# Kernel optimization log

Measured on AMD Instinct MI355X. Metric: run time of the kernel, lower is better.

Reference implementation:

```python
import jax, jax.numpy as jnp
import numpy as np

N = 100000
E = 1600000
D_IN = 128
D_OUT = 128
HEADS = 4
C = D_OUT // HEADS  # per-head channels = 32
NEG_SLOPE = 0.2
EPS_SOFTMAX = 1e-16
EPS_LN = 1e-5


def setup_inputs() -> dict:
    key = jax.random.key(0)
    ks = jax.random.split(key, 10)
    x = jax.random.normal(ks[0], (N, D_IN), dtype=jnp.float32)
    edge_index = jax.random.randint(ks[1], (2, E), 0, N, dtype=jnp.int64)
    s = 1.0 / np.sqrt(D_IN)
    W = jax.random.normal(ks[2], (D_IN, HEADS * C), dtype=jnp.float32) * s
    att_src = jax.random.normal(ks[3], (HEADS, C), dtype=jnp.float32) * (1.0 / np.sqrt(C))
    att_dst = jax.random.normal(ks[4], (HEADS, C), dtype=jnp.float32) * (1.0 / np.sqrt(C))
    gat_bias = jax.random.normal(ks[5], (D_OUT,), dtype=jnp.float32) * 0.02
    skip_W = jax.random.normal(ks[6], (D_IN, D_OUT), dtype=jnp.float32) * s
    skip_b = jax.random.normal(ks[7], (D_OUT,), dtype=jnp.float32) * 0.02
    ln_g = jnp.ones((D_OUT,), dtype=jnp.float32)
    ln_b = jnp.zeros((D_OUT,), dtype=jnp.float32)
    return {"x": x, "edge_index": edge_index, "W": W, "att_src": att_src,
            "att_dst": att_dst, "gat_bias": gat_bias, "skip_W": skip_W,
            "skip_b": skip_b, "ln_g": ln_g, "ln_b": ln_b}


def _gat_edge_conv(x, src, dst, W, att_src, att_dst, gat_bias, skip_W, skip_b, ln_g, ln_b):
    n = x.shape[0]
    h = (x @ W).reshape(n, HEADS, C)                      # [N,H,C]
    a_s = jnp.einsum('nhc,hc->nh', h, att_src)            # [N,H]
    a_d = jnp.einsum('nhc,hc->nh', h, att_dst)            # [N,H]
    e = jax.nn.leaky_relu(a_s[src] + a_d[dst], NEG_SLOPE)  # [E,H]
    # segment softmax over incoming edges of each dst node
    m = jax.ops.segment_max(e, dst, num_segments=n)        # [N,H]
    p = jnp.exp(e - m[dst])
    z = jax.ops.segment_sum(p, dst, num_segments=n)        # [N,H]
    alpha = p / (z[dst] + EPS_SOFTMAX)                     # [E,H]
    msg = h[src] * alpha[:, :, None]                       # [E,H,C]
    out = jax.ops.segment_sum(msg, dst, num_segments=n)    # [N,H,C]
    out = out.reshape(n, HEADS * C) + gat_bias
    out = out + x @ skip_W + skip_b
    mu = out.mean(-1, keepdims=True)
    var = ((out - mu) ** 2).mean(-1, keepdims=True)
    return (out - mu) * jax.lax.rsqrt(var + EPS_LN) * ln_g + ln_b


def reference(x, edge_index, W, att_src, att_dst, gat_bias, skip_W, skip_b, ln_g, ln_b):
    n = x.shape[0]
    loops = jnp.arange(n, dtype=edge_index.dtype)          # PyG GATConv add_self_loops=True
    src = jnp.concatenate([edge_index[0], loops])
    dst = jnp.concatenate([edge_index[1], loops])
    return _gat_edge_conv(x, src, dst, W, att_src, att_dst, gat_bias, skip_W, skip_b, ln_g, ln_b)
```

## Files before the change

kernel.cpp:

```cpp
#include <hip/hip_runtime.h>
#include <hip/hip_bf16.h>

#define D 128
#define HEADS 4
#define NEG_SLOPE 0.2f

typedef __attribute__((ext_vector_type(8))) short short8;
typedef __attribute__((ext_vector_type(4))) float f32x4;

__device__ __forceinline__ float lrelu(float v) {
    return v > 0.f ? v : NEG_SLOPE * v;
}

__device__ __forceinline__ short f2bf(float v) {
    __hip_bfloat16 b = __float2bfloat16(v);
    short s;
    __builtin_memcpy(&s, &b, 2);
    return s;
}

__device__ __forceinline__ float bf_lo(unsigned int u) {
    return __uint_as_float(u << 16);
}
__device__ __forceinline__ float bf_hi(unsigned int u) {
    return __uint_as_float(u & 0xffff0000u);
}

__global__ __launch_bounds__(256)
void wprep_kernel(const float* __restrict__ W, const float* __restrict__ S,
                  short* __restrict__ wsT) {
    int idx = blockIdx.x * 256 + threadIdx.x;
    int nn = idx >> 7, k = idx & 127;
    float v = (nn < 128) ? W[k * D + nn] : S[k * D + (nn - 128)];
    wsT[idx] = f2bf(v);
}

#define LDSPAD 136
__global__ __launch_bounds__(512, 4)
void gemm_mfma_kernel(const float* __restrict__ x, const short* __restrict__ wsT,
                      const float* __restrict__ skip_b, const float* __restrict__ gat_bias,
                      unsigned short* __restrict__ hb, unsigned short* __restrict__ baseb,
                      int n) {
    __shared__ short xs[64][LDSPAD];
    const int t = threadIdx.x;
    const int row0 = blockIdx.x * 64;
    #pragma unroll
    for (int i = 0; i < 4; ++i) {
        int f = t + 512 * i;
        int row = f >> 5, c4 = (f & 31) * 4;
        float4 v = make_float4(0.f, 0.f, 0.f, 0.f);
        if (row0 + row < n) v = *(const float4*)&x[(size_t)(row0 + row) * D + c4];
        short4 s4;
        s4.x = f2bf(v.x); s4.y = f2bf(v.y); s4.z = f2bf(v.z); s4.w = f2bf(v.w);
        *(short4*)&xs[row][c4] = s4;
    }
    __syncthreads();
    const int wv = t >> 6, lane = t & 63;
    const int lo = lane & 15, hi = lane >> 4;
    const int wr = wv >> 2;
    const int wc = wv & 3;
    f32x4 acc[2][4] = {};
    #pragma unroll
    for (int k0 = 0; k0 < 128; k0 += 32) {
        const int kk = k0 + hi * 8;
        short8 a0 = *(const short8*)&xs[wr * 32 + lo][kk];
        short8 a1 = *(const short8*)&xs[wr * 32 + 16 + lo][kk];
        #pragma unroll
        for (int nt = 0; nt < 4; ++nt) {
            short8 b = *(const short8*)&wsT[(wc * 64 + nt * 16 + lo) * D + kk];
            acc[0][nt] = __builtin_amdgcn_mfma_f32_16x16x32_bf16(a0, b, acc[0][nt], 0, 0, 0);
            acc[1][nt] = __builtin_amdgcn_mfma_f32_16x16x32_bf16(a1, b, acc[1][nt], 0, 0, 0);
        }
    }
    #pragma unroll
    for (int nt = 0; nt < 4; ++nt) {
        const int cc = wc * 64 + nt * 16 + lo;
        const bool isH = cc < 128;
        const float bb = isH ? 0.f : (skip_b[cc - 128] + gat_bias[cc - 128]);
        unsigned short* dst = isH ? hb : baseb;
        const int c = isH ? cc : cc - 128;
        #pragma unroll
        for (int mt = 0; mt < 2; ++mt) {
            const int rbase = row0 + wr * 32 + mt * 16 + hi * 4;
            #pragma unroll
            for (int reg = 0; reg < 4; ++reg) {
                const int r = rbase + reg;
                if (r < n) dst[(size_t)r * D + c] = (unsigned short)f2bf(acc[mt][nt][reg] + bb);
            }
        }
    }
}

__global__ __launch_bounds__(128)
void attn_proj_kernel(const unsigned short* __restrict__ hb,
                      const float* __restrict__ att_src, const float* __restrict__ att_dst,
                      float* __restrict__ a_s, float* __restrict__ a_d, int n) {
    const int i = blockIdx.x;
    const int j = threadIdx.x;
    float hv = __uint_as_float(((unsigned int)hb[(size_t)i * D + j]) << 16);
    float ps = hv * att_src[j];
    float pd = hv * att_dst[j];
    #pragma unroll
    for (int off = 16; off; off >>= 1) {
        ps += __shfl_down(ps, off, 32);
        pd += __shfl_down(pd, off, 32);
    }
    __shared__ float sa[HEADS], sd[HEADS];
    if ((j & 31) == 0) { sa[j >> 5] = ps; sd[j >> 5] = pd; }
    __syncthreads();
    if (j < HEADS) {
        a_s[i * HEADS + j] = sa[j];
        a_d[i * HEADS + j] = sd[j];
    }
}

#define BEPT 16
#define BCHUNK (256 * BEPT)

__global__ __launch_bounds__(256)
void bhist_kernel(const int* __restrict__ ei, int* __restrict__ bcnt, int E_, int nb) {
    __shared__ int hist[512];
    const int t = threadIdx.x;
    for (int q = t; q < 512; q += 256) hist[q] = 0;
    __syncthreads();
    const int base = blockIdx.x * BCHUNK;
    #pragma unroll
    for (int i = 0; i < BEPT; ++i) {
        int e = base + i * 256 + t;
        if (e < E_) atomicAdd(&hist[ei[E_ + e] >> 8], 1);
    }
    __syncthreads();
    for (int q = t; q < nb; q += 256) {
        int v = hist[q];
        if (v) atomicAdd(&bcnt[q], v);
    }
}

__global__ __launch_bounds__(512)
void bscan_kernel(const int* __restrict__ bcnt, int* __restrict__ bbase,
                  int* __restrict__ woffA, int nb) {
    __shared__ int ts[512];
    const int t = threadIdx.x;
    int v = (t < nb) ? bcnt[t] : 0;
    ts[t] = v;
    __syncthreads();
    for (int off = 1; off < 512; off <<= 1) {
        int x = (t >= off) ? ts[t - off] : 0;
        __syncthreads();
        ts[t] += x;
        __syncthreads();
    }
    if (t < nb) {
        int ex = ts[t] - v;
        bbase[t] = ex;
        woffA[t] = ex;
        if (t == nb - 1) bbase[nb] = ts[t];
    }
}

__global__ __launch_bounds__(256)
void binA_kernel(const int* __restrict__ ei, int* __restrict__ woffA,
                 int2* __restrict__ pairs, int E_, int nb) {
    __shared__ int hist[512];
    __shared__ int gbase[512];
    const int t = threadIdx.x;
    for (int q = t; q < 512; q += 256) hist[q] = 0;
    __syncthreads();
    int sv[BEPT], dv[BEPT], rk[BEPT];
    const int base = blockIdx.x * BCHUNK;
    #pragma unroll
    for (int i = 0; i < BEPT; ++i) {
        int e = base + i * 256 + t;
        if (e < E_) {
            sv[i] = ei[e];
            dv[i] = ei[E_ + e];
            rk[i] = atomicAdd(&hist[dv[i] >> 8], 1);
        } else {
            sv[i] = -1;
        }
    }
    __syncthreads();
    for (int q = t; q < nb; q += 256) {
        int v = hist[q];
        gbase[q] = v ? atomicAdd(&woffA[q], v) : 0;
    }
    __syncthreads();
    #pragma unroll
    for (int i = 0; i < BEPT; ++i) {
        if (sv[i] >= 0) {
            int pos = gbase[dv[i] >> 8] + rk[i];
            pairs[pos] = make_int2(sv[i], dv[i]);
        }
    }
}

__global__ __launch_bounds__(256)
void binB_kernel(const int2* __restrict__ pairs, const int* __restrict__ bbase,
                 int* __restrict__ cnt, int* __restrict__ offs,
                 int* __restrict__ ssrc, int n) {
    __shared__ int nhist[256];
    __shared__ int sc[256];
    __shared__ int run[256];
    const int b = blockIdx.x;
    const int t = threadIdx.x;
    const int node0 = b << 8;
    const int sbeg = bbase[b], send = bbase[b + 1];
    nhist[t] = 0;
    __syncthreads();
    for (int e = sbeg + t; e < send; e += 256)
        atomicAdd(&nhist[pairs[e].y - node0], 1);
    __syncthreads();
    int v = nhist[t];
    sc[t] = v;
    __syncthreads();
    for (int off = 1; off < 256; off <<= 1) {
        int x = (t >= off) ? sc[t - off] : 0;
        __syncthreads();
        sc[t] += x;
        __syncthreads();
    }
    int ex = sc[t] - v;
    run[t] = sbeg + ex;
    if (node0 + t < n) {
        cnt[node0 + t] = v;
        offs[node0 + t] = sbeg + ex;
    }
    __syncthreads();
    for (int e = sbeg + t; e < send; e += 256) {
        int2 p = pairs[e];
        int pos = atomicAdd(&run[p.y - node0], 1);
        ssrc[pos] = p.x;
    }
}

__global__ __launch_bounds__(256)
void gather_kernel(const int* __restrict__ offs, const int* __restrict__ cnt,
                   const int* __restrict__ ssrc, const float* __restrict__ a_s,
                   const float* __restrict__ a_d, const unsigned int* __restrict__ hb2,
                   const unsigned int* __restrict__ baseb2,
                   const float* __restrict__ ln_g, const float* __restrict__ ln_b,
                   float* __restrict__ out, int n) {
    const int lane = threadIdx.x & 63;
    const int i = blockIdx.x * 4 + (threadIdx.x >> 6);
    if (i >= n) return;
    const int e4 = lane >> 2, h4 = lane & 3;
    const int hA = lane >> 4;
    const float as_h4 = a_s[i * HEADS + h4];
    const float ad_h4 = a_d[i * HEADS + h4];
    float qself = __expf(lrelu(as_h4 + ad_h4));
    float zacc = (e4 == 0) ? qself : 0.f;
    float qselfA = __shfl(qself, hA, 64);
    unsigned int hv0 = hb2[(size_t)i * 64 + lane];
    float acc0 = bf_lo(hv0) * qselfA;
    float acc1 = bf_hi(hv0) * qselfA;
    const int o = offs[i];
    const int c = cnt[i];
    for (int k0 = 0; k0 < c; k0 += 16) {
        const int rem = c - k0;
        int sidx = 0;
        float q = 0.f;
        if (e4 < rem) {
            sidx = ssrc[o + k0 + e4];
            q = __expf(lrelu(a_s[sidx * HEADS + h4] + ad_h4));
        }
        zacc += q;
        const int m = rem < 16 ? rem : 16;
        int ee = 0;
        for (; ee + 4 <= m; ee += 4) {
            const int s0 = __shfl(sidx, (ee + 0) * 4, 64);
            const int s1 = __shfl(sidx, (ee + 1) * 4, 64);
            const int s2 = __shfl(sidx, (ee + 2) * 4, 64);
            const int s3 = __shfl(sidx, (ee + 3) * 4, 64);
            const float q0 = __shfl(q, (ee + 0) * 4 + hA, 64);
            const float q1 = __shfl(q, (ee + 1) * 4 + hA, 64);
            const float q2 = __shfl(q, (ee + 2) * 4 + hA, 64);
            const float q3 = __shfl(q, (ee + 3) * 4 + hA, 64);
            const unsigned int v0 = hb2[(size_t)s0 * 64 + lane];
            const unsigned int v1 = hb2[(size_t)s1 * 64 + lane];
            const unsigned int v2 = hb2[(size_t)s2 * 64 + lane];
            const unsigned int v3 = hb2[(size_t)s3 * 64 + lane];
            acc0 = fmaf(bf_lo(v0), q0, acc0);
            acc1 = fmaf(bf_hi(v0), q0, acc1);
            acc0 = fmaf(bf_lo(v1), q1, acc0);
            acc1 = fmaf(bf_hi(v1), q1, acc1);
            acc0 = fmaf(bf_lo(v2), q2, acc0);
            acc1 = fmaf(bf_hi(v2), q2, acc1);
            acc0 = fmaf(bf_lo(v3), q3, acc0);
            acc1 = fmaf(bf_hi(v3), q3, acc1);
        }
        for (; ee < m; ++ee) {
            const int s = __shfl(sidx, ee * 4, 64);
            const float qq = __shfl(q, ee * 4 + hA, 64);
            const unsigned int v = hb2[(size_t)s * 64 + lane];
            acc0 = fmaf(bf_lo(v), qq, acc0);
            acc1 = fmaf(bf_hi(v), qq, acc1);
        }
    }
    #pragma unroll
    for (int off = 4; off < 64; off <<= 1) zacc += __shfl_xor(zacc, off, 64);
    const float zz = __shfl(zacc, hA, 64);
    const float rz = 1.f / (zz + 1e-16f);
    const unsigned int bv = baseb2[(size_t)i * 64 + lane];
    float v0 = acc0 * rz + bf_lo(bv);
    float v1 = acc1 * rz + bf_hi(bv);
    float s1 = v0 + v1, s2 = v0 * v0 + v1 * v1;
    #pragma unroll
    for (int off = 1; off < 64; off <<= 1) {
        s1 += __shfl_xor(s1, off, 64);
        s2 += __shfl_xor(s2, off, 64);
    }
    const float mu = s1 * (1.f / 128.f);
    const float var = s2 * (1.f / 128.f) - mu * mu;
    const float r = rsqrtf(var + 1e-5f);
    const float2 g2 = *(const float2*)&ln_g[2 * lane];
    const float2 b2 = *(const float2*)&ln_b[2 * lane];
    float2 o2;
    o2.x = (v0 - mu) * r * g2.x + b2.x;
    o2.y = (v1 - mu) * r * g2.y + b2.y;
    *(float2*)&out[(size_t)i * D + 2 * lane] = o2;
}

extern "C" void kernel_launch(void* const* d_in, const int* in_sizes, int n_in,
                              void* d_out, int out_size, void* d_ws, size_t ws_size,
                              hipStream_t stream) {
    const float* x        = (const float*)d_in[0];
    const int*   ei       = (const int*)d_in[1];
    const float* W        = (const float*)d_in[2];
    const float* att_src  = (const float*)d_in[3];
    const float* att_dst  = (const float*)d_in[4];
    const float* gat_bias = (const float*)d_in[5];
    const float* skip_W   = (const float*)d_in[6];
    const float* skip_b   = (const float*)d_in[7];
    const float* ln_g     = (const float*)d_in[8];
    const float* ln_b     = (const float*)d_in[9];
    float* out = (float*)d_out;

    const int n  = in_sizes[0] / D;
    const int E_ = in_sizes[1] / 2;
    const int nb = (n + 255) >> 8;

    char* p = (char*)d_ws;
    auto carve = [&p](size_t bytes) {
        char* r = p;
        p += (bytes + 255) & ~(size_t)255;
        return r;
    };
    short* wsT            = (short*)carve(32768 * sizeof(short));
    unsigned short* hb    = (unsigned short*)carve((size_t)n * D * 2);
    unsigned short* baseb = (unsigned short*)carve((size_t)n * D * 2);
    float* a_s            = (float*)carve((size_t)n * HEADS * 4);
    float* a_d            = (float*)carve((size_t)n * HEADS * 4);
    int*   cnt            = (int*)carve((size_t)n * 4);
    int*   offs           = (int*)carve((size_t)n * 4);
    int*   bcnt           = (int*)carve(512 * 4);
    int*   bbase          = (int*)carve(513 * 4);
    int*   woffA          = (int*)carve(512 * 4);
    int*   ssrc           = (int*)carve((size_t)E_ * 4);
    int2*  pairs          = (int2*)carve((size_t)E_ * 8);

    hipMemsetAsync(bcnt, 0, 512 * sizeof(int), stream);

    wprep_kernel<<<128, 256, 0, stream>>>(W, skip_W, wsT);
    gemm_mfma_kernel<<<(n + 63) / 64, 512, 0, stream>>>(x, wsT, skip_b, gat_bias,
                                                        hb, baseb, n);
    attn_proj_kernel<<<n, 128, 0, stream>>>(hb, att_src, att_dst, a_s, a_d, n);
    const int BA = (E_ + BCHUNK - 1) / BCHUNK;
    bhist_kernel<<<BA, 256, 0, stream>>>(ei, bcnt, E_, nb);
    bscan_kernel<<<1, 512, 0, stream>>>(bcnt, bbase, woffA, nb);
    binA_kernel<<<BA, 256, 0, stream>>>(ei, woffA, pairs, E_, nb);
    binB_kernel<<<nb, 256, 0, stream>>>(pairs, bbase, cnt, offs, ssrc, n);
    gather_kernel<<<(n + 3) / 4, 256, 0, stream>>>(offs, cnt, ssrc, a_s, a_d,
                                                   (const unsigned int*)hb,
                                                   (const unsigned int*)baseb,
                                                   ln_g, ln_b, out, n);
}
```

Before: 319.5 us.

## Split wave into two half-wave edge streams with 8-byte gathers; batch attention projection

The gather kernel now has each half-wave (32 lanes) process alternate edges. Each lane loads 8 bytes (4 bf16 channels) per neighbour row, so one wavefront fetches two neighbour rows per load instruction, and the halves are combined with a cross-half shuffle at the end. The attention projection kernel now processes 4 nodes per 256-thread block, one wave per node, using xor-shuffles instead of shared memory and a syncthreads. This cuts load-instruction count and per-edge shuffle overhead in the memory-bound gather. The cost is an extra reduction across the two halves, and only half the lanes stay active for the final store.

```diff
diff --git a/kernel.cpp b/kernel.cpp
--- a/kernel.cpp
+++ b/kernel.cpp
@@ -91,26 +91,27 @@
     }
 }
 
-__global__ __launch_bounds__(128)
-void attn_proj_kernel(const unsigned short* __restrict__ hb,
+__global__ __launch_bounds__(256)
+void attn_proj_kernel(const unsigned int* __restrict__ hb2,
                       const float* __restrict__ att_src, const float* __restrict__ att_dst,
                       float* __restrict__ a_s, float* __restrict__ a_d, int n) {
-    const int i = blockIdx.x;
-    const int j = threadIdx.x;
-    float hv = __uint_as_float(((unsigned int)hb[(size_t)i * D + j]) << 16);
-    float ps = hv * att_src[j];
-    float pd = hv * att_dst[j];
-    #pragma unroll
-    for (int off = 16; off; off >>= 1) {
-        ps += __shfl_down(ps, off, 32);
-        pd += __shfl_down(pd, off, 32);
-    }
-    __shared__ float sa[HEADS], sd[HEADS];
-    if ((j & 31) == 0) { sa[j >> 5] = ps; sd[j >> 5] = pd; }
-    __syncthreads();
-    if (j < HEADS) {
-        a_s[i * HEADS + j] = sa[j];
-        a_d[i * HEADS + j] = sd[j];
+    const int lane = threadIdx.x & 63;
+    const int i = blockIdx.x * 4 + (threadIdx.x >> 6);
+    if (i >= n) return;
+    unsigned int u = hb2[(size_t)i * 64 + lane];
+    float h0 = bf_lo(u), h1 = bf_hi(u);
+    float2 as2 = ((const float2*)att_src)[lane];
+    float2 ad2 = ((const float2*)att_dst)[lane];
+    float ps = h0 * as2.x + h1 * as2.y;
+    float pd = h0 * ad2.x + h1 * ad2.y;
+    #pragma unroll
+    for (int off = 1; off < 16; off <<= 1) {
+        ps += __shfl_xor(ps, off, 64);
+        pd += __shfl_xor(pd, off, 64);
+    }
+    if ((lane & 15) == 0) {
+        a_s[i * HEADS + (lane >> 4)] = ps;
+        a_d[i * HEADS + (lane >> 4)] = pd;
     }
 }
 
@@ -236,23 +237,31 @@
 __global__ __launch_bounds__(256)
 void gather_kernel(const int* __restrict__ offs, const int* __restrict__ cnt,
                    const int* __restrict__ ssrc, const float* __restrict__ a_s,
-                   const float* __restrict__ a_d, const unsigned int* __restrict__ hb2,
-                   const unsigned int* __restrict__ baseb2,
+                   const float* __restrict__ a_d, const uint2* __restrict__ hb4,
+                   const uint2* __restrict__ baseb4,
                    const float* __restrict__ ln_g, const float* __restrict__ ln_b,
                    float* __restrict__ out, int n) {
     const int lane = threadIdx.x & 63;
     const int i = blockIdx.x * 4 + (threadIdx.x >> 6);
     if (i >= n) return;
     const int e4 = lane >> 2, h4 = lane & 3;
-    const int hA = lane >> 4;
+    const int l31 = lane & 31;
+    const int myhead = l31 >> 3;
+    const int esel = (lane < 32) ? 0 : 1;
     const float as_h4 = a_s[i * HEADS + h4];
     const float ad_h4 = a_d[i * HEADS + h4];
     float qself = __expf(lrelu(as_h4 + ad_h4));
     float zacc = (e4 == 0) ? qself : 0.f;
-    float qselfA = __shfl(qself, hA, 64);
-    unsigned int hv0 = hb2[(size_t)i * 64 + lane];
-    float acc0 = bf_lo(hv0) * qselfA;
-    float acc1 = bf_hi(hv0) * qselfA;
+    float acc0, acc1, acc2, acc3;
+    {
+        uint2 u = hb4[(size_t)i * 32 + l31];
+        float qs = __shfl(qself, myhead, 64);
+        float w = (lane < 32) ? qs : 0.f;
+        acc0 = bf_lo(u.x) * w;
+        acc1 = bf_hi(u.x) * w;
+        acc2 = bf_lo(u.y) * w;
+        acc3 = bf_hi(u.y) * w;
+    }
     const int o = offs[i];
     const int c = cnt[i];
     for (int k0 = 0; k0 < c; k0 += 16) {
@@ -266,58 +275,84 @@
         zacc += q;
         const int m = rem < 16 ? rem : 16;
         int ee = 0;
-        for (; ee + 4 <= m; ee += 4) {
-            const int s0 = __shfl(sidx, (ee + 0) * 4, 64);
-            const int s1 = __shfl(sidx, (ee + 1) * 4, 64);
-            const int s2 = __shfl(sidx, (ee + 2) * 4, 64);
-            const int s3 = __shfl(sidx, (ee + 3) * 4, 64);
-            const float q0 = __shfl(q, (ee + 0) * 4 + hA, 64);
-            const float q1 = __shfl(q, (ee + 1) * 4 + hA, 64);
-            const float q2 = __shfl(q, (ee + 2) * 4 + hA, 64);
-            const float q3 = __shfl(q, (ee + 3) * 4 + hA, 64);
-            const unsigned int v0 = hb2[(size_t)s0 * 64 + lane];
-            const unsigned int v1 = hb2[(size_t)s1 * 64 + lane];
-            const unsigned int v2 = hb2[(size_t)s2 * 64 + lane];
-            const unsigned int v3 = hb2[(size_t)s3 * 64 + lane];
-            acc0 = fmaf(bf_lo(v0), q0, acc0);
-            acc1 = fmaf(bf_hi(v0), q0, acc1);
-            acc0 = fmaf(bf_lo(v1), q1, acc0);
-            acc1 = fmaf(bf_hi(v1), q1, acc1);
-            acc0 = fmaf(bf_lo(v2), q2, acc0);
-            acc1 = fmaf(bf_hi(v2), q2, acc1);
-            acc0 = fmaf(bf_lo(v3), q3, acc0);
-            acc1 = fmaf(bf_hi(v3), q3, acc1);
-        }
-        for (; ee < m; ++ee) {
-            const int s = __shfl(sidx, ee * 4, 64);
-            const float qq = __shfl(q, ee * 4 + hA, 64);
-            const unsigned int v = hb2[(size_t)s * 64 + lane];
-            acc0 = fmaf(bf_lo(v), qq, acc0);
-            acc1 = fmaf(bf_hi(v), qq, acc1);
-        }
-    }
+        for (; ee + 8 <= m; ee += 8) {
+            const int sl0 = (ee + 0 + esel) * 4;
+            const int sl1 = (ee + 2 + esel) * 4;
+            const int sl2 = (ee + 4 + esel) * 4;
+            const int sl3 = (ee + 6 + esel) * 4;
+            const int sA = __shfl(sidx, sl0, 64);
+            const int sB = __shfl(sidx, sl1, 64);
+            const int sC = __shfl(sidx, sl2, 64);
+            const int sD = __shfl(sidx, sl3, 64);
+            const float qA = __shfl(q, sl0 + myhead, 64);
+            const float qB = __shfl(q, sl1 + myhead, 64);
+            const float qC = __shfl(q, sl2 + myhead, 64);
+            const float qD = __shfl(q, sl3 + myhead, 64);
+            const uint2 uA = hb4[(size_t)sA * 32 + l31];
+            const uint2 uB = hb4[(size_t)sB * 32 + l31];
+            const uint2 uC = hb4[(size_t)sC * 32 + l31];
+            const uint2 uD = hb4[(size_t)sD * 32 + l31];
+            acc0 = fmaf(bf_lo(uA.x), qA, acc0);
+            acc1 = fmaf(bf_hi(uA.x), qA, acc1);
+            acc2 = fmaf(bf_lo(uA.y), qA, acc2);
+            acc3 = fmaf(bf_hi(uA.y), qA, acc3);
+            acc0 = fmaf(bf_lo(uB.x), qB, acc0);
+            acc1 = fmaf(bf_hi(uB.x), qB, acc1);
+            acc2 = fmaf(bf_lo(uB.y), qB, acc2);
+            acc3 = fmaf(bf_hi(uB.y), qB, acc3);
+            acc0 = fmaf(bf_lo(uC.x), qC, acc0);
+            acc1 = fmaf(bf_hi(uC.x), qC, acc1);
+            acc2 = fmaf(bf_lo(uC.y), qC, acc2);
+            acc3 = fmaf(bf_hi(uC.y), qC, acc3);
+            acc0 = fmaf(bf_lo(uD.x), qD, acc0);
+            acc1 = fmaf(bf_hi(uD.x), qD, acc1);
+            acc2 = fmaf(bf_lo(uD.y), qD, acc2);
+            acc3 = fmaf(bf_hi(uD.y), qD, acc3);
+        }
+        for (; ee < m; ee += 2) {
+            const int sl = (ee + esel) * 4;
+            const int sA = __shfl(sidx, sl, 64);
+            const float qA = __shfl(q, sl + myhead, 64);
+            const uint2 uA = hb4[(size_t)sA * 32 + l31];
+            acc0 = fmaf(bf_lo(uA.x), qA, acc0);
+            acc1 = fmaf(bf_hi(uA.x), qA, acc1);
+            acc2 = fmaf(bf_lo(uA.y), qA, acc2);
+            acc3 = fmaf(bf_hi(uA.y), qA, acc3);
+        }
+    }
+    acc0 += __shfl_xor(acc0, 32, 64);
+    acc1 += __shfl_xor(acc1, 32, 64);
+    acc2 += __shfl_xor(acc2, 32, 64);
+    acc3 += __shfl_xor(acc3, 32, 64);
     #pragma unroll
     for (int off = 4; off < 64; off <<= 1) zacc += __shfl_xor(zacc, off, 64);
-    const float zz = __shfl(zacc, hA, 64);
+    const float zz = __shfl(zacc, myhead, 64);
     const float rz = 1.f / (zz + 1e-16f);
-    const unsigned int bv = baseb2[(size_t)i * 64 + lane];
-    float v0 = acc0 * rz + bf_lo(bv);
-    float v1 = acc1 * rz + bf_hi(bv);
-    float s1 = v0 + v1, s2 = v0 * v0 + v1 * v1;
-    #pragma unroll
-    for (int off = 1; off < 64; off <<= 1) {
+    const uint2 bv = baseb4[(size_t)i * 32 + l31];
+    float v0 = acc0 * rz + bf_lo(bv.x);
+    float v1 = acc1 * rz + bf_hi(bv.x);
+    float v2 = acc2 * rz + bf_lo(bv.y);
+    float v3 = acc3 * rz + bf_hi(bv.y);
+    float s1 = v0 + v1 + v2 + v3;
+    float s2 = v0 * v0 + v1 * v1 + v2 * v2 + v3 * v3;
+    #pragma unroll
+    for (int off = 1; off < 32; off <<= 1) {
         s1 += __shfl_xor(s1, off, 64);
         s2 += __shfl_xor(s2, off, 64);
     }
     const float mu = s1 * (1.f / 128.f);
     const float var = s2 * (1.f / 128.f) - mu * mu;
     const float r = rsqrtf(var + 1e-5f);
-    const float2 g2 = *(const float2*)&ln_g[2 * lane];
-    const float2 b2 = *(const float2*)&ln_b[2 * lane];
-    float2 o2;
-    o2.x = (v0 - mu) * r * g2.x + b2.x;
-    o2.y = (v1 - mu) * r * g2.y + b2.y;
-    *(float2*)&out[(size_t)i * D + 2 * lane] = o2;
+    if (lane < 32) {
+        const float4 g4 = ((const float4*)ln_g)[l31];
+        const float4 b4 = ((const float4*)ln_b)[l31];
+        float4 o4;
+        o4.x = (v0 - mu) * r * g4.x + b4.x;
+        o4.y = (v1 - mu) * r * g4.y + b4.y;
+        o4.z = (v2 - mu) * r * g4.z + b4.z;
+        o4.w = (v3 - mu) * r * g4.w + b4.w;
+        ((float4*)out)[(size_t)i * 32 + l31] = o4;
+    }
 }
 
 extern "C" void kernel_launch(void* const* d_in, const int* in_sizes, int n_in,
@@ -363,14 +398,15 @@
     wprep_kernel<<<128, 256, 0, stream>>>(W, skip_W, wsT);
     gemm_mfma_kernel<<<(n + 63) / 64, 512, 0, stream>>>(x, wsT, skip_b, gat_bias,
                                                         hb, baseb, n);
-    attn_proj_kernel<<<n, 128, 0, stream>>>(hb, att_src, att_dst, a_s, a_d, n);
+    attn_proj_kernel<<<(n + 3) / 4, 256, 0, stream>>>((const unsigned int*)hb,
+                                                      att_src, att_dst, a_s, a_d, n);
     const int BA = (E_ + BCHUNK - 1) / BCHUNK;
     bhist_kernel<<<BA, 256, 0, stream>>>(ei, bcnt, E_, nb);
     bscan_kernel<<<1, 512, 0, stream>>>(bcnt, bbase, woffA, nb);
     binA_kernel<<<BA, 256, 0, stream>>>(ei, woffA, pairs, E_, nb);
     binB_kernel<<<nb, 256, 0, stream>>>(pairs, bbase, cnt, offs, ssrc, n);
     gather_kernel<<<(n + 3) / 4, 256, 0, stream>>>(offs, cnt, ssrc, a_s, a_d,
-                                                   (const unsigned int*)hb,
-                                                   (const unsigned int*)baseb,
+                                                   (const uint2*)hb,
+                                                   (const uint2*)baseb,
                                                    ln_g, ln_b, out, n);
 }
```

After: 304.6 us. -4.7%, faster.
